# Performance work log

Measured on AMD Instinct MI355X. Metric: run time of the kernel, lower is better.

Reference implementation:

```python
import jax, jax.numpy as jnp
import numpy as np


def setup_inputs() -> dict:
    key = jax.random.key(0)
    k1, k2, k3, k4, k5, k6, k7 = jax.random.split(key, 7)
    B, N, E = 8, 8192, 65536
    Dn, De = 64, 64            # node_shape, edge_shape
    IU = 128                   # input_units
    Dc = 2 * Dn + De           # concat dim = 192
    nodes = jax.random.normal(k1, (B, N, Dn), dtype=jnp.float32)
    edges = jax.random.normal(k2, (B, E, De), dtype=jnp.float32)
    senders = jax.random.randint(k3, (B, E), 0, N, dtype=jnp.int32)
    receivers = jax.random.randint(k4, (B, E), 0, N, dtype=jnp.int32)
    s_in = 1.0 / np.sqrt(Dc)
    s_out = 1.0 / np.sqrt(IU)
    s_edge = 1.0 / np.sqrt(Dn)
    W_in = jax.random.uniform(k5, (Dc, IU), jnp.float32, -s_in, s_in)
    b_in = jnp.zeros((IU,), jnp.float32)
    W_out = jax.random.uniform(k6, (IU, Dn), jnp.float32, -s_out, s_out)
    b_out = jnp.zeros((Dn,), jnp.float32)
    W_edge = jax.random.uniform(k7, (Dn, De), jnp.float32, -s_edge, s_edge)
    b_edge = jnp.zeros((De,), jnp.float32)
    return {"nodes": nodes, "edges": edges, "senders": senders, "receivers": receivers,
            "W_in": W_in, "b_in": b_in, "W_out": W_out, "b_out": b_out,
            "W_edge": W_edge, "b_edge": b_edge}


def reference(nodes, edges, senders, receivers, W_in, b_in, W_out, b_out, W_edge, b_edge):
    B, N, Dn = nodes.shape
    E = edges.shape[1]
    De = edges.shape[2]
    # per-graph offsets so indices address the flattened [B*N] node table
    offsets = (jnp.arange(B, dtype=senders.dtype) * N)[:, None]          # [B,1]
    s_flat = senders.reshape(-1)                                         # [B*E]
    r_flat = receivers.reshape(-1)
    s_off = jnp.where(s_flat != -1, s_flat + jnp.broadcast_to(offsets, (B, E)).reshape(-1), s_flat)
    r_off = jnp.where(r_flat != -1, r_flat + jnp.broadcast_to(offsets, (B, E)).reshape(-1), r_flat)
    nodes_flat = nodes.reshape(B * N, Dn)
    edges_flat = edges.reshape(B * E, De)
    # gather node features onto edges: [recv || edge || send]
    concat = jnp.concatenate([nodes_flat[r_off], edges_flat, nodes_flat[s_off]], axis=1)  # [B*E, 2Dn+De]
    h = jax.nn.relu(concat @ W_in + b_in)            # node_layer_in
    e_new = jax.nn.relu(h @ W_out + b_out)           # node_layer_out -> [B*E, Dn]
    # unsorted_segment_mean over receivers (empty segments -> 0, as in TF)
    sums = jax.ops.segment_sum(e_new, r_off, num_segments=B * N)         # [B*N, Dn]
    counts = jax.ops.segment_sum(jnp.ones((B * E,), e_new.dtype), r_off, num_segments=B * N)
    nodes_new = jnp.where(counts[:, None] > 0, sums / jnp.maximum(counts, 1.0)[:, None], 0.0)
    edges_out = jax.nn.relu(e_new @ W_edge + b_edge)  # edge_layer -> [B*E, De]
    return (nodes_new.reshape(B, N, Dn), edges_out.reshape(B, E, De), s_flat, r_flat)
```

## Files before the change

kernel.cpp:

```cpp
#include <hip/hip_runtime.h>

typedef __attribute__((ext_vector_type(8))) __bf16 bf16x8;
typedef __attribute__((ext_vector_type(4))) __bf16 bf16x4;
typedef __attribute__((ext_vector_type(4))) float f32x4;

constexpr int kB = 8, kN = 8192, kE = 65536;
constexpr int kBN = kB * kN;
constexpr int kBE = kB * kE;
constexpr int kDN = 64, kDE = 64, kIU = 128;

constexpr int XS = 200;
constexpr int HS = 136;
constexpr int ES = 72;

__device__ __forceinline__ void lds_barrier() {
    asm volatile("s_waitcnt lgkmcnt(0)\n\ts_barrier" ::: "memory");
}

__device__ __forceinline__ void atomic_pk_add_bf16(__bf16* p, uint32_t pk) {
    const unsigned long long a64 = (unsigned long long)p;
    asm volatile("global_atomic_pk_add_bf16 %0, %1, off sc1"
                 :: "v"(a64), "v"(pk) : "memory");
}

__global__ __launch_bounds__(256, 3)
void edge_mlp_pk(const float* __restrict__ nodes,
                 const float* __restrict__ edges,
                 const int* __restrict__ senders,
                 const int* __restrict__ receivers,
                 const float* __restrict__ W_in,
                 const float* __restrict__ b_in,
                 const float* __restrict__ W_out,
                 const float* __restrict__ b_out,
                 const float* __restrict__ W_edge,
                 const float* __restrict__ b_edge,
                 float* __restrict__ edges_out,
                 float* __restrict__ out_sf,
                 float* __restrict__ out_rf,
                 __bf16* __restrict__ sums,
                 float* __restrict__ counts)
{
    __shared__ alignas(16) __bf16 Xs_[64 * XS];
    __shared__ alignas(16) __bf16 Hs_[64 * HS];
    __shared__ alignas(16) __bf16 Es_[64 * ES];
    __shared__ int rsS[2][64];

    const int tid  = threadIdx.x;
    const int lane = tid & 63;
    const int wave = tid >> 6;
    const int c16  = lane & 15;
    const int q    = lane >> 4;

    bf16x8 winf[6][2];
#pragma unroll
    for (int kk = 0; kk < 6; ++kk)
#pragma unroll
        for (int nt = 0; nt < 2; ++nt)
#pragma unroll
            for (int j = 0; j < 8; ++j)
                winf[kk][nt][j] =
                    (__bf16)W_in[(kk * 32 + q * 8 + j) * kIU + wave * 32 + nt * 16 + c16];
    bf16x8 woutf[4];
#pragma unroll
    for (int kk = 0; kk < 4; ++kk)
#pragma unroll
        for (int j = 0; j < 8; ++j)
            woutf[kk][j] = (__bf16)W_out[(kk * 32 + q * 8 + j) * kDN + wave * 16 + c16];
    bf16x8 wedgef[2];
#pragma unroll
    for (int kk = 0; kk < 2; ++kk)
#pragma unroll
        for (int j = 0; j < 8; ++j)
            wedgef[kk][j] = (__bf16)W_edge[(kk * 32 + q * 8 + j) * kDE + wave * 16 + c16];

    const float bin0 = b_in[wave * 32 + c16];
    const float bin1 = b_in[wave * 32 + 16 + c16];
    const float bo   = b_out[wave * 16 + c16];
    const float beg  = b_edge[wave * 16 + c16];

    const int row = tid >> 2;
    const int qt  = tid & 3;
    const int ntiles = kBE / 64;
    const int stride = gridDim.x;

    int t = blockIdx.x;
    int rV, sV, rN, sN;
    float4 G[12];
    {
        const int g = t * 64 + row;
        rV = receivers[g]; sV = senders[g];
        const int b  = g >> 16;
        const int rg = (rV < 0) ? (kBN - 1) : rV + (b << 13);
        const int sg = (sV < 0) ? (kBN - 1) : sV + (b << 13);
        const float4* nrec = (const float4*)nodes + (size_t)rg * 16;
        const float4* ez   = (const float4*)edges + (size_t)g * 16;
        const float4* nsnd = (const float4*)nodes + (size_t)sg * 16;
#pragma unroll
        for (int i = 0; i < 4; ++i) {
            G[i] = nrec[qt + 4 * i]; G[4 + i] = ez[qt + 4 * i]; G[8 + i] = nsnd[qt + 4 * i];
        }
        const int t1 = (t + stride < ntiles) ? (t + stride) : t;
        const int g1 = t1 * 64 + row;
        rN = receivers[g1]; sN = senders[g1];
    }

    int buf = 0;
    for (; t < ntiles; t += stride) {
        const int g0 = t * 64;

        {
            const int b  = (g0 + row) >> 16;
            const int rs = (rV < 0) ? -1 : rV + (b << 13);
            if (qt == 0) {
                rsS[buf][row] = rs;
                const int g = g0 + row;
                out_sf[g] = (float)sV;
                out_rf[g] = (float)rV;
                if (rs >= 0) atomicAdd(&counts[rs], 1.0f);
            }
            __bf16* xr = &Xs_[row * XS];
#pragma unroll
            for (int i = 0; i < 4; ++i) {
                const int c = 4 * qt + 16 * i;
                float4 a = G[i], e = G[4 + i], s = G[8 + i];
                *(bf16x4*)&xr[c]       = (bf16x4){(__bf16)a.x,(__bf16)a.y,(__bf16)a.z,(__bf16)a.w};
                *(bf16x4*)&xr[64 + c]  = (bf16x4){(__bf16)e.x,(__bf16)e.y,(__bf16)e.z,(__bf16)e.w};
                *(bf16x4*)&xr[128 + c] = (bf16x4){(__bf16)s.x,(__bf16)s.y,(__bf16)s.z,(__bf16)s.w};
            }
        }
        lds_barrier();

        {
            const int rG = rN, sG = sN;
            const int tn = (t + stride < ntiles) ? (t + stride) : t;
            const int gn = tn * 64 + row;
            const int b  = gn >> 16;
            const int rg = (rG < 0) ? (kBN - 1) : rG + (b << 13);
            const int sg = (sG < 0) ? (kBN - 1) : sG + (b << 13);
            const float4* nrec = (const float4*)nodes + (size_t)rg * 16;
            const float4* ez   = (const float4*)edges + (size_t)gn * 16;
            const float4* nsnd = (const float4*)nodes + (size_t)sg * 16;
#pragma unroll
            for (int i = 0; i < 4; ++i) {
                G[i] = nrec[qt + 4 * i]; G[4 + i] = ez[qt + 4 * i]; G[8 + i] = nsnd[qt + 4 * i];
            }
            const int t2 = (t + 2 * stride < ntiles) ? (t + 2 * stride) : tn;
            const int g2 = t2 * 64 + row;
            rN = receivers[g2]; sN = senders[g2];
            rV = rG; sV = sG;
        }

#pragma unroll
        for (int m = 0; m < 4; ++m) {
            const __bf16* ar = &Xs_[(m * 16 + c16) * XS + q * 8];
            bf16x8 a[6];
#pragma unroll
            for (int kk = 0; kk < 6; ++kk) a[kk] = *(const bf16x8*)(ar + kk * 32);
            f32x4 acc0 = (f32x4){0.f,0.f,0.f,0.f}, acc1 = (f32x4){0.f,0.f,0.f,0.f};
#pragma unroll
            for (int kk = 0; kk < 6; ++kk)
                acc0 = __builtin_amdgcn_mfma_f32_16x16x32_bf16(a[kk], winf[kk][0], acc0, 0, 0, 0);
#pragma unroll
            for (int kk = 0; kk < 6; ++kk)
                acc1 = __builtin_amdgcn_mfma_f32_16x16x32_bf16(a[kk], winf[kk][1], acc1, 0, 0, 0);
#pragma unroll
            for (int r = 0; r < 4; ++r) {
                __bf16* hr = &Hs_[(m * 16 + q * 4 + r) * HS + wave * 32];
                hr[c16]      = (__bf16)fmaxf(acc0[r] + bin0, 0.f);
                hr[16 + c16] = (__bf16)fmaxf(acc1[r] + bin1, 0.f);
            }
        }
        lds_barrier();

#pragma unroll
        for (int m = 0; m < 4; ++m) {
            const __bf16* ar = &Hs_[(m * 16 + c16) * HS + q * 8];
            bf16x8 a[4];
#pragma unroll
            for (int kk = 0; kk < 4; ++kk) a[kk] = *(const bf16x8*)(ar + kk * 32);
            f32x4 acc = (f32x4){0.f,0.f,0.f,0.f};
#pragma unroll
            for (int kk = 0; kk < 4; ++kk)
                acc = __builtin_amdgcn_mfma_f32_16x16x32_bf16(a[kk], woutf[kk], acc, 0, 0, 0);
#pragma unroll
            for (int r = 0; r < 4; ++r)
                Es_[(m * 16 + q * 4 + r) * ES + wave * 16 + c16] = (__bf16)fmaxf(acc[r] + bo, 0.f);
        }
        lds_barrier();

#pragma unroll
        for (int m = 0; m < 4; ++m) {
            const __bf16* ar = &Es_[(m * 16 + c16) * ES + q * 8];
            bf16x8 a0 = *(const bf16x8*)ar;
            bf16x8 a1 = *(const bf16x8*)(ar + 32);
            f32x4 acc = (f32x4){0.f,0.f,0.f,0.f};
            acc = __builtin_amdgcn_mfma_f32_16x16x32_bf16(a0, wedgef[0], acc, 0, 0, 0);
            acc = __builtin_amdgcn_mfma_f32_16x16x32_bf16(a1, wedgef[1], acc, 0, 0, 0);
#pragma unroll
            for (int r = 0; r < 4; ++r)
                edges_out[(size_t)(g0 + m * 16 + q * 4 + r) * kDE + wave * 16 + c16] =
                    fmaxf(acc[r] + beg, 0.f);
        }

        {
            const int half = lane >> 5;
            const int pc   = lane & 31;
#pragma unroll
            for (int i = 0; i < 8; ++i) {
                const int rr = wave * 16 + half * 8 + i;
                const int rs = rsS[buf][rr];
                if (rs >= 0) {
                    const uint32_t pk = *(const uint32_t*)&Es_[rr * ES + pc * 2];
                    atomic_pk_add_bf16(sums + (size_t)rs * kDN + pc * 2, pk);
                }
            }
        }
        buf ^= 1;
    }
}

__global__ __launch_bounds__(256)
void finalize_kernel(const unsigned int* __restrict__ sums_u32,
                     const float* __restrict__ counts,
                     float* __restrict__ out)
{
    const int t = blockIdx.x * blockDim.x + threadIdx.x;
    const unsigned int p0 = sums_u32[t * 2];
    const unsigned int p1 = sums_u32[t * 2 + 1];
    const float c = counts[t >> 4];
    float4 o;
    if (c > 0.f) {
        const float inv = 1.f / c;
        union { unsigned int u; float f; } v;
        v.u = p0 << 16;            o.x = v.f * inv;
        v.u = p0 & 0xffff0000u;    o.y = v.f * inv;
        v.u = p1 << 16;            o.z = v.f * inv;
        v.u = p1 & 0xffff0000u;    o.w = v.f * inv;
    } else {
        o.x = o.y = o.z = o.w = 0.f;
    }
    ((float4*)out)[t] = o;
}

extern "C" void kernel_launch(void* const* d_in, const int* in_sizes, int n_in,
                              void* d_out, int out_size, void* d_ws, size_t ws_size,
                              hipStream_t stream) {
    const float* nodes     = (const float*)d_in[0];
    const float* edges     = (const float*)d_in[1];
    const int*   senders   = (const int*)d_in[2];
    const int*   receivers = (const int*)d_in[3];
    const float* W_in      = (const float*)d_in[4];
    const float* b_in      = (const float*)d_in[5];
    const float* W_out     = (const float*)d_in[6];
    const float* b_out     = (const float*)d_in[7];
    const float* W_edge    = (const float*)d_in[8];
    const float* b_edge    = (const float*)d_in[9];

    float* out       = (float*)d_out;
    float* edges_out = out + (size_t)kBN * kDN;
    float* out_sf    = edges_out + (size_t)kBE * kDE;
    float* out_rf    = out_sf + kBE;

    __bf16* sums  = (__bf16*)d_ws;
    float* counts = (float*)((char*)d_ws + (size_t)kBN * kDN * 2);

    hipMemsetAsync(d_ws, 0, (size_t)kBN * kDN * 2 + (size_t)kBN * 4, stream);

    edge_mlp_pk<<<2048, 256, 0, stream>>>(
        nodes, edges, senders, receivers,
        W_in, b_in, W_out, b_out, W_edge, b_edge,
        edges_out, out_sf, out_rf, sums, counts);

    finalize_kernel<<<kBN * kDN / 4 / 256, 256, 0, stream>>>(
        (const unsigned int*)sums, counts, out);
}
```

Measured before the change: 374.8 us.

## Pre-cast node table to bf16 and double-buffer gather registers across two tiles

A new pre-pass kernel converts the node feature table to bf16 and stores it in the output buffer as scratch, which halves the bytes moved by the random receiver and sender gathers. The main loop is restructured into two register sets so each tile's gather is issued two tiles ahead, giving more latency hiding. The cost is an extra kernel launch plus a full read and write of the node table, and higher register pressure from holding two gather sets, which could lower occupancy under launch_bounds(256,3). Reusing the output region as scratch relies on finalize overwriting it later.

```diff
diff --git a/kernel.cpp b/kernel.cpp
--- a/kernel.cpp
+++ b/kernel.cpp
@@ -23,8 +23,127 @@
                  :: "v"(a64), "v"(pk) : "memory");
 }
 
+__global__ __launch_bounds__(256)
+void cast_nodes(const float* __restrict__ nodes, __bf16* __restrict__ nbf) {
+    const int t = blockIdx.x * 256 + threadIdx.x;
+    const float4* nf = (const float4*)nodes;
+    const float4 a = nf[t * 2];
+    const float4 c = nf[t * 2 + 1];
+    bf16x8 o = {(__bf16)a.x, (__bf16)a.y, (__bf16)a.z, (__bf16)a.w,
+                (__bf16)c.x, (__bf16)c.y, (__bf16)c.z, (__bf16)c.w};
+    ((bf16x8*)nbf)[t] = o;
+}
+
+
+#define GATHER(Rr, Sr, Ee, tg, rv, sv) do {                                   \
+    const int g_ = (tg) * 64 + row;                                           \
+    const int b_ = g_ >> 16;                                                  \
+    const int rg_ = ((rv) < 0) ? (kBN - 1) : (rv) + (b_ << 13);               \
+    const int sg_ = ((sv) < 0) ? (kBN - 1) : (sv) + (b_ << 13);               \
+    const bf16x8* nb_ = (const bf16x8*)nbf;                                   \
+    Rr[0] = nb_[rg_ * 8 + qt * 2];  Rr[1] = nb_[rg_ * 8 + qt * 2 + 1];        \
+    Sr[0] = nb_[sg_ * 8 + qt * 2];  Sr[1] = nb_[sg_ * 8 + qt * 2 + 1];        \
+    const float4* ez_ = (const float4*)edges + (size_t)g_ * 16;               \
+    Ee[0] = ez_[qt];  Ee[1] = ez_[qt + 4];                                    \
+    Ee[2] = ez_[qt + 8];  Ee[3] = ez_[qt + 12];                               \
+} while (0)
+
+#define STAGE(Rr, Sr, Ee, tg, rv, sv, bufi) do {                              \
+    const int g_ = (tg) * 64 + row;                                           \
+    const int b_ = g_ >> 16;                                                  \
+    const int rs_ = ((rv) < 0) ? -1 : (rv) + (b_ << 13);                      \
+    if (qt == 0) {                                                            \
+        rsS[bufi][row] = rs_;                                                 \
+        out_sf[g_] = (float)(sv);                                             \
+        out_rf[g_] = (float)(rv);                                             \
+        if (rs_ >= 0) atomicAdd(&counts[rs_], 1.0f);                          \
+    }                                                                         \
+    __bf16* xr_ = &Xs_[row * XS];                                             \
+    \
+    *(bf16x8*)&xr_[qt * 16]           = Rr[0];                                \
+    *(bf16x8*)&xr_[qt * 16 + 8]       = Rr[1];                                \
+    *(bf16x8*)&xr_[128 + qt * 16]     = Sr[0];                                \
+    *(bf16x8*)&xr_[128 + qt * 16 + 8] = Sr[1];                                \
+    _Pragma("unroll")                                                         \
+    for (int i_ = 0; i_ < 4; ++i_) {                                          \
+        float4 e_ = Ee[i_];                                                   \
+        *(bf16x4*)&xr_[64 + 4 * qt + 16 * i_] =                               \
+            (bf16x4){(__bf16)e_.x, (__bf16)e_.y, (__bf16)e_.z, (__bf16)e_.w}; \
+    }                                                                         \
+} while (0)
+
+#define COMPUTE(tg, bufi) do {                                                \
+    const int g0_ = (tg) * 64;                                                \
+    _Pragma("unroll")                                                         \
+    for (int m_ = 0; m_ < 4; ++m_) {                                          \
+        const __bf16* ar_ = &Xs_[(m_ * 16 + c16) * XS + q * 8];               \
+        bf16x8 a_[6];                                                         \
+        _Pragma("unroll")                                                     \
+        for (int kk_ = 0; kk_ < 6; ++kk_)                                     \
+            a_[kk_] = *(const bf16x8*)(ar_ + kk_ * 32);                       \
+        f32x4 acc0_ = (f32x4){0.f, 0.f, 0.f, 0.f};                            \
+        f32x4 acc1_ = (f32x4){0.f, 0.f, 0.f, 0.f};                            \
+        _Pragma("unroll")                                                     \
+        for (int kk_ = 0; kk_ < 6; ++kk_)                                     \
+            acc0_ = __builtin_amdgcn_mfma_f32_16x16x32_bf16(a_[kk_], winf[kk_][0], acc0_, 0, 0, 0); \
+        _Pragma("unroll")                                                     \
+        for (int kk_ = 0; kk_ < 6; ++kk_)                                     \
+            acc1_ = __builtin_amdgcn_mfma_f32_16x16x32_bf16(a_[kk_], winf[kk_][1], acc1_, 0, 0, 0); \
+        _Pragma("unroll")                                                     \
+        for (int r_ = 0; r_ < 4; ++r_) {                                      \
+            __bf16* hr_ = &Hs_[(m_ * 16 + q * 4 + r_) * HS + wave * 32];      \
+            hr_[c16]      = (__bf16)fmaxf(acc0_[r_] + bin0, 0.f);             \
+            hr_[16 + c16] = (__bf16)fmaxf(acc1_[r_] + bin1, 0.f);             \
+        }                                                                     \
+    }                                                                         \
+    lds_barrier();                                           \
+    _Pragma("unroll")                                                         \
+    for (int m_ = 0; m_ < 4; ++m_) {                                          \
+        const __bf16* ar_ = &Hs_[(m_ * 16 + c16) * HS + q * 8];               \
+        bf16x8 a_[4];                                                         \
+        _Pragma("unroll")                                                     \
+        for (int kk_ = 0; kk_ < 4; ++kk_)                                     \
+            a_[kk_] = *(const bf16x8*)(ar_ + kk_ * 32);                       \
+        f32x4 acc_ = (f32x4){0.f, 0.f, 0.f, 0.f};                             \
+        _Pragma("unroll")                                                     \
+        for (int kk_ = 0; kk_ < 4; ++kk_)                                     \
+            acc_ = __builtin_amdgcn_mfma_f32_16x16x32_bf16(a_[kk_], woutf[kk_], acc_, 0, 0, 0); \
+        _Pragma("unroll")                                                     \
+        for (int r_ = 0; r_ < 4; ++r_)                                        \
+            Es_[(m_ * 16 + q * 4 + r_) * ES + wave * 16 + c16] =              \
+                (__bf16)fmaxf(acc_[r_] + bo, 0.f);                            \
+    }                                                                         \
+    lds_barrier();                                           \
+    _Pragma("unroll")                                                         \
+    for (int m_ = 0; m_ < 4; ++m_) {                                          \
+        const __bf16* ar_ = &Es_[(m_ * 16 + c16) * ES + q * 8];               \
+        bf16x8 a0_ = *(const bf16x8*)ar_;                                     \
+        bf16x8 a1_ = *(const bf16x8*)(ar_ + 32);                              \
+        f32x4 acc_ = (f32x4){0.f, 0.f, 0.f, 0.f};                             \
+        acc_ = __builtin_amdgcn_mfma_f32_16x16x32_bf16(a0_, wedgef[0], acc_, 0, 0, 0); \
+        acc_ = __builtin_amdgcn_mfma_f32_16x16x32_bf16(a1_, wedgef[1], acc_, 0, 0, 0); \
+        _Pragma("unroll")                                                     \
+        for (int r_ = 0; r_ < 4; ++r_)                                        \
+            edges_out[(size_t)(g0_ + m_ * 16 + q * 4 + r_) * kDE + wave * 16 + c16] = \
+                fmaxf(acc_[r_] + beg, 0.f);                                   \
+    }                                                                         \
+    {                                                                         \
+        const int half_ = lane >> 5;                                          \
+        const int pc_   = lane & 31;                                          \
+        _Pragma("unroll")                                                     \
+        for (int i_ = 0; i_ < 8; ++i_) {                                      \
+            const int rr_ = wave * 16 + half_ * 8 + i_;                       \
+            const int rs2_ = rsS[bufi][rr_];                                  \
+            if (rs2_ >= 0) {                                                  \
+                const uint32_t pk_ = *(const uint32_t*)&Es_[rr_ * ES + pc_ * 2]; \
+                atomic_pk_add_bf16(sums + (size_t)rs2_ * kDN + pc_ * 2, pk_); \
+            }                                                                 \
+        }                                                                     \
+    }                                                                         \
+} while (0)
+
 __global__ __launch_bounds__(256, 3)
-void edge_mlp_pk(const float* __restrict__ nodes,
+void edge_mlp_pk(const __bf16* __restrict__ nbf,
                  const float* __restrict__ edges,
                  const int* __restrict__ senders,
                  const int* __restrict__ receivers,
@@ -80,142 +199,56 @@
 
     const int row = tid >> 2;
     const int qt  = tid & 3;
-    const int ntiles = kBE / 64;
-    const int stride = gridDim.x;
-
-    int t = blockIdx.x;
-    int rV, sV, rN, sN;
-    float4 G[12];
+    constexpr int ntiles = kBE / 64;
+    const int S = gridDim.x;
+
+    bf16x8 R0[2], Sd0[2]; float4 E0[4]; int rV0, sV0;
+    bf16x8 R1[2], Sd1[2]; float4 E1[4]; int rV1, sV1;
+    int rI = 0, sI = 0;
+
+    const int t0 = blockIdx.x;
     {
-        const int g = t * 64 + row;
-        rV = receivers[g]; sV = senders[g];
-        const int b  = g >> 16;
-        const int rg = (rV < 0) ? (kBN - 1) : rV + (b << 13);
-        const int sg = (sV < 0) ? (kBN - 1) : sV + (b << 13);
-        const float4* nrec = (const float4*)nodes + (size_t)rg * 16;
-        const float4* ez   = (const float4*)edges + (size_t)g * 16;
-        const float4* nsnd = (const float4*)nodes + (size_t)sg * 16;
-#pragma unroll
-        for (int i = 0; i < 4; ++i) {
-            G[i] = nrec[qt + 4 * i]; G[4 + i] = ez[qt + 4 * i]; G[8 + i] = nsnd[qt + 4 * i];
+        const int g = t0 * 64 + row;
+        rV0 = receivers[g]; sV0 = senders[g];
+    }
+    if (t0 + S < ntiles) {
+        const int g = (t0 + S) * 64 + row;
+        rV1 = receivers[g]; sV1 = senders[g];
+    } else { rV1 = 0; sV1 = 0; }
+    GATHER(R0, Sd0, E0, t0, rV0, sV0);
+    if (t0 + S < ntiles) GATHER(R1, Sd1, E1, t0 + S, rV1, sV1);
+    if (t0 + 2 * S < ntiles) {
+        const int g = (t0 + 2 * S) * 64 + row;
+        rI = receivers[g]; sI = senders[g];
+    }
+
+    for (int t = t0; t < ntiles; t += 2 * S) {
+        STAGE(R0, Sd0, E0, t, rV0, sV0, 0);
+        lds_barrier();
+        if (t + 2 * S < ntiles) {
+            GATHER(R0, Sd0, E0, t + 2 * S, rI, sI);
+            rV0 = rI; sV0 = sI;
         }
-        const int t1 = (t + stride < ntiles) ? (t + stride) : t;
-        const int g1 = t1 * 64 + row;
-        rN = receivers[g1]; sN = senders[g1];
-    }
-
-    int buf = 0;
-    for (; t < ntiles; t += stride) {
-        const int g0 = t * 64;
-
-        {
-            const int b  = (g0 + row) >> 16;
-            const int rs = (rV < 0) ? -1 : rV + (b << 13);
-            if (qt == 0) {
-                rsS[buf][row] = rs;
-                const int g = g0 + row;
-                out_sf[g] = (float)sV;
-                out_rf[g] = (float)rV;
-                if (rs >= 0) atomicAdd(&counts[rs], 1.0f);
+        if (t + 3 * S < ntiles) {
+            const int g = (t + 3 * S) * 64 + row;
+            rI = receivers[g]; sI = senders[g];
+        }
+        COMPUTE(t, 0);
+
+        const int tB = t + S;
+        if (tB < ntiles) {
+            STAGE(R1, Sd1, E1, tB, rV1, sV1, 1);
+            lds_barrier();
+            if (t + 3 * S < ntiles) {
+                GATHER(R1, Sd1, E1, t + 3 * S, rI, sI);
+                rV1 = rI; sV1 = sI;
             }
-            __bf16* xr = &Xs_[row * XS];
-#pragma unroll
-            for (int i = 0; i < 4; ++i) {
-                const int c = 4 * qt + 16 * i;
-                float4 a = G[i], e = G[4 + i], s = G[8 + i];
-                *(bf16x4*)&xr[c]       = (bf16x4){(__bf16)a.x,(__bf16)a.y,(__bf16)a.z,(__bf16)a.w};
-                *(bf16x4*)&xr[64 + c]  = (bf16x4){(__bf16)e.x,(__bf16)e.y,(__bf16)e.z,(__bf16)e.w};
-                *(bf16x4*)&xr[128 + c] = (bf16x4){(__bf16)s.x,(__bf16)s.y,(__bf16)s.z,(__bf16)s.w};
+            if (t + 4 * S < ntiles) {
+                const int g = (t + 4 * S) * 64 + row;
+                rI = receivers[g]; sI = senders[g];
             }
+            COMPUTE(tB, 1);
         }
-        lds_barrier();
-
-        {
-            const int rG = rN, sG = sN;
-            const int tn = (t + stride < ntiles) ? (t + stride) : t;
-            const int gn = tn * 64 + row;
-            const int b  = gn >> 16;
-            const int rg = (rG < 0) ? (kBN - 1) : rG + (b << 13);
-            const int sg = (sG < 0) ? (kBN - 1) : sG + (b << 13);
-            const float4* nrec = (const float4*)nodes + (size_t)rg * 16;
-            const float4* ez   = (const float4*)edges + (size_t)gn * 16;
-            const float4* nsnd = (const float4*)nodes + (size_t)sg * 16;
-#pragma unroll
-            for (int i = 0; i < 4; ++i) {
-                G[i] = nrec[qt + 4 * i]; G[4 + i] = ez[qt + 4 * i]; G[8 + i] = nsnd[qt + 4 * i];
-            }
-            const int t2 = (t + 2 * stride < ntiles) ? (t + 2 * stride) : tn;
-            const int g2 = t2 * 64 + row;
-            rN = receivers[g2]; sN = senders[g2];
-            rV = rG; sV = sG;
-        }
-
-#pragma unroll
-        for (int m = 0; m < 4; ++m) {
-            const __bf16* ar = &Xs_[(m * 16 + c16) * XS + q * 8];
-            bf16x8 a[6];
-#pragma unroll
-            for (int kk = 0; kk < 6; ++kk) a[kk] = *(const bf16x8*)(ar + kk * 32);
-            f32x4 acc0 = (f32x4){0.f,0.f,0.f,0.f}, acc1 = (f32x4){0.f,0.f,0.f,0.f};
-#pragma unroll
-            for (int kk = 0; kk < 6; ++kk)
-                acc0 = __builtin_amdgcn_mfma_f32_16x16x32_bf16(a[kk], winf[kk][0], acc0, 0, 0, 0);
-#pragma unroll
-            for (int kk = 0; kk < 6; ++kk)
-                acc1 = __builtin_amdgcn_mfma_f32_16x16x32_bf16(a[kk], winf[kk][1], acc1, 0, 0, 0);
-#pragma unroll
-            for (int r = 0; r < 4; ++r) {
-                __bf16* hr = &Hs_[(m * 16 + q * 4 + r) * HS + wave * 32];
-                hr[c16]      = (__bf16)fmaxf(acc0[r] + bin0, 0.f);
-                hr[16 + c16] = (__bf16)fmaxf(acc1[r] + bin1, 0.f);
-            }
-        }
-        lds_barrier();
-
-#pragma unroll
-        for (int m = 0; m < 4; ++m) {
-            const __bf16* ar = &Hs_[(m * 16 + c16) * HS + q * 8];
-            bf16x8 a[4];
-#pragma unroll
-            for (int kk = 0; kk < 4; ++kk) a[kk] = *(const bf16x8*)(ar + kk * 32);
-            f32x4 acc = (f32x4){0.f,0.f,0.f,0.f};
-#pragma unroll
-            for (int kk = 0; kk < 4; ++kk)
-                acc = __builtin_amdgcn_mfma_f32_16x16x32_bf16(a[kk], woutf[kk], acc, 0, 0, 0);
-#pragma unroll
-            for (int r = 0; r < 4; ++r)
-                Es_[(m * 16 + q * 4 + r) * ES + wave * 16 + c16] = (__bf16)fmaxf(acc[r] + bo, 0.f);
-        }
-        lds_barrier();
-
-#pragma unroll
-        for (int m = 0; m < 4; ++m) {
-            const __bf16* ar = &Es_[(m * 16 + c16) * ES + q * 8];
-            bf16x8 a0 = *(const bf16x8*)ar;
-            bf16x8 a1 = *(const bf16x8*)(ar + 32);
-            f32x4 acc = (f32x4){0.f,0.f,0.f,0.f};
-            acc = __builtin_amdgcn_mfma_f32_16x16x32_bf16(a0, wedgef[0], acc, 0, 0, 0);
-            acc = __builtin_amdgcn_mfma_f32_16x16x32_bf16(a1, wedgef[1], acc, 0, 0, 0);
-#pragma unroll
-            for (int r = 0; r < 4; ++r)
-                edges_out[(size_t)(g0 + m * 16 + q * 4 + r) * kDE + wave * 16 + c16] =
-                    fmaxf(acc[r] + beg, 0.f);
-        }
-
-        {
-            const int half = lane >> 5;
-            const int pc   = lane & 31;
-#pragma unroll
-            for (int i = 0; i < 8; ++i) {
-                const int rr = wave * 16 + half * 8 + i;
-                const int rs = rsS[buf][rr];
-                if (rs >= 0) {
-                    const uint32_t pk = *(const uint32_t*)&Es_[rr * ES + pc * 2];
-                    atomic_pk_add_bf16(sums + (size_t)rs * kDN + pc * 2, pk);
-                }
-            }
-        }
-        buf ^= 1;
     }
 }
 
@@ -264,10 +297,14 @@
     __bf16* sums  = (__bf16*)d_ws;
     float* counts = (float*)((char*)d_ws + (size_t)kBN * kDN * 2);
 
+    __bf16* nbf = (__bf16*)out;
+
     hipMemsetAsync(d_ws, 0, (size_t)kBN * kDN * 2 + (size_t)kBN * 4, stream);
 
+    cast_nodes<<<kBN * kDN / 8 / 256, 256, 0, stream>>>(nodes, nbf);
+
     edge_mlp_pk<<<2048, 256, 0, stream>>>(
-        nodes, edges, senders, receivers,
+        nbf, edges, senders, receivers,
         W_in, b_in, W_out, b_out, W_edge, b_edge,
         edges_out, out_sf, out_rf, sums, counts);
 
```

After: 433.5 us. +15.7%, slower.
